# Optimization experiments

Hardware: AMD Instinct MI355X
Metric: run time of the kernel (lower is better)

Reference implementation:

```python
import jax, jax.numpy as jnp
import numpy as np

B, S, IN, H = 16, 1024, 1024, 1024

def setup_inputs() -> dict:
    key = jax.random.key(0)
    k1, k2 = jax.random.split(key)
    x = jax.random.normal(k1, (B, S, IN), dtype=jnp.float32)
    # xavier_uniform with gain sqrt(2) over shape [2H, IN]
    limit = np.sqrt(2.0) * np.sqrt(6.0 / (2 * H + IN))
    W = jax.random.uniform(k2, (2 * H, IN), dtype=jnp.float32, minval=-limit, maxval=limit)
    return {"x": x, "W": W}

def reference(x, W):
    # i = x @ W.T -> [B, S, 2H]; split into key/value pre-activations
    i = jnp.einsum('bsi,oi->bso', x, W)
    ik, iv = jnp.split(i, 2, axis=2)          # each [B, S, H]
    mem0 = jnp.zeros((x.shape[0], H, H), dtype=x.dtype)

    def step(mem, kv):
        ik_t, iv_t = kv                        # [B, H] each
        k = jax.nn.relu(ik_t)
        v = jax.nn.relu(iv_t)
        # Hebbian plasticity rule: delta_mem = key outer val
        mem = mem + jnp.einsum('bk,bv->bkv', k, v)
        return mem, (k, v)

    # scan over time: move seq axis to front
    kv_seq = (jnp.swapaxes(ik, 0, 1), jnp.swapaxes(iv, 0, 1))  # [S, B, H]
    mem, (keys, vals) = jax.lax.scan(step, mem0, kv_seq)
    keys = jnp.swapaxes(keys, 0, 1)            # [B, S, H]
    vals = jnp.swapaxes(vals, 0, 1)
    return mem, keys, vals
```

## Files before the change

kernel.cpp:

```cpp
#include <hip/hip_runtime.h>

#define B_  16
#define S_  1024
#define IN_ 1024
#define H_  1024
#define N1  (2*H_)
#define M1  (B_*S_)
#define K1  IN_
#define XN  (M1*IN_)
#define WN  (N1*IN_)
#define LDG 1024

#define BM  256
#define BN  256
#define BK  64
#define CP  257

#define USZ  8192
#define ASZ  16384
#define TBUF 32768

typedef __attribute__((ext_vector_type(8))) short  short8;
typedef __attribute__((ext_vector_type(4))) float  floatx4;

__device__ __forceinline__ unsigned short f2bf(float f) {
    unsigned int u = __float_as_uint(f);
    u += 0x7fffu + ((u >> 16) & 1u);
    return (unsigned short)(u >> 16);
}

#define GLDS16(gp, lp) __builtin_amdgcn_global_load_lds(                      \
    (const __attribute__((address_space(1))) void*)(gp),                      \
    (__attribute__((address_space(3))) void*)(lp), 16, 0, 0)

#define WAITVM(N) { asm volatile("s_waitcnt vmcnt(" #N ")" ::: "memory");     \
                    __builtin_amdgcn_s_barrier();                             \
                    __builtin_amdgcn_sched_barrier(0); }

__global__ __launch_bounds__(256) void convert_kernel(
    const float* __restrict__ x, const float* __restrict__ W,
    unsigned short* __restrict__ xb, unsigned short* __restrict__ Wb)
{
    size_t i = ((size_t)blockIdx.x * 256 + threadIdx.x) * 8;
    const float* src;
    unsigned short* dst;
    if (i < (size_t)XN) { src = x + i; dst = xb + i; }
    else                { src = W + (i - XN); dst = Wb + (i - XN); }
    float4 a = *(const float4*)(src);
    float4 b = *(const float4*)(src + 4);
    ushort4 p = { f2bf(a.x), f2bf(a.y), f2bf(a.z), f2bf(a.w) };
    ushort4 q = { f2bf(b.x), f2bf(b.y), f2bf(b.z), f2bf(b.w) };
    *(ushort4*)(dst)     = p;
    *(ushort4*)(dst + 4) = q;
}

__device__ __forceinline__ void stage_u(
    const unsigned short* Ag, const unsigned short* Bg,
    unsigned short* buf, int op, int kh, int kt, int wave, int lane)
{
    const unsigned short* src = op ? Bg : Ag;
    unsigned short* dst = buf + op * ASZ + kh * USZ;
#pragma unroll
    for (int h = 0; h < 2; ++h) {
        int e   = (wave * 2 + h) * 64 + lane;
        int row = e >> 2, p = e & 3;
        int c   = p ^ (row & 3);
        GLDS16(src + (size_t)row * LDG + kt + kh * 32 + c * 8,
               dst + (wave * 2 + h) * 512);
    }
}

__device__ __forceinline__ void half_tile(
    const unsigned short* bufc, floatx4 (&acc)[8][4], int kc,
    const unsigned short* Ag, const unsigned short* Bg,
    unsigned short* bufn, int ktn, bool st,
    int wave, int lane, int wmw, int wnw, int quad, int r)
{
    const unsigned short* cA = bufc + kc * USZ;
    const unsigned short* cB = bufc + ASZ + kc * USZ;
    const int sw = (quad ^ (r & 3)) * 8;
    short8 bfr[4];
#pragma unroll
    for (int j = 0; j < 4; ++j)
        bfr[j] = *(const short8*)(cB + (wnw + j * 16 + r) * 32 + sw);
#pragma unroll
    for (int mh = 0; mh < 2; ++mh) {
        short8 af[4];
#pragma unroll
        for (int i = 0; i < 4; ++i)
            af[i] = *(const short8*)(cA + (wmw + (mh * 4 + i) * 16 + r) * 32 + sw);
        if (st) stage_u(Ag, Bg, bufn, mh, kc, ktn, wave, lane);
        __builtin_amdgcn_s_setprio(1);
#pragma unroll
        for (int i = 0; i < 4; ++i)
#pragma unroll
            for (int j = 0; j < 4; ++j)
                acc[mh * 4 + i][j] = __builtin_amdgcn_mfma_f32_16x16x32_bf16(
                    af[i], bfr[j], acc[mh * 4 + i][j], 0, 0, 0);
        __builtin_amdgcn_s_setprio(0);
    }
}

__device__ __forceinline__ void gemm_core(
    const unsigned short* Ag, const unsigned short* Bg,
    unsigned short* lds, floatx4 (&acc)[8][4], int wave, int lane)
{
    const int quad = lane >> 4, r = lane & 15;
    const int wmw  = (wave >> 2) * 128;
    const int wnw  = (wave & 3) * 64;

    stage_u(Ag, Bg, lds, 0, 0, 0, wave, lane);
    stage_u(Ag, Bg, lds, 1, 0, 0, wave, lane);
    stage_u(Ag, Bg, lds, 0, 1, 0, wave, lane);
    stage_u(Ag, Bg, lds, 1, 1, 0, wave, lane);

    for (int t = 0; t < 15; ++t) {
        unsigned short* bufc = lds + (t & 1) * TBUF;
        unsigned short* bufn = lds + ((t + 1) & 1) * TBUF;
        const int ktn = (t + 1) * BK;
        WAITVM(4)
        half_tile(bufc, acc, 0, Ag, Bg, bufn, ktn, true, wave, lane, wmw, wnw, quad, r);
        WAITVM(4)
        half_tile(bufc, acc, 1, Ag, Bg, bufn, ktn, true, wave, lane, wmw, wnw, quad, r);
    }
    {
        unsigned short* bufc = lds + TBUF;
        WAITVM(4)
        half_tile(bufc, acc, 0, Ag, Bg, bufc, 0, false, wave, lane, wmw, wnw, quad, r);
        WAITVM(0)
        half_tile(bufc, acc, 1, Ag, Bg, bufc, 0, false, wave, lane, wmw, wnw, quad, r);
    }
    __syncthreads();
}

__global__ __launch_bounds__(512, 2) void gemm1_kernel(
    const unsigned short* __restrict__ xb, const unsigned short* __restrict__ Wb,
    float* __restrict__ out,
    unsigned short* __restrict__ kT, unsigned short* __restrict__ vT)
{
    __shared__ unsigned short lds[65536];

    const int tid  = threadIdx.x;
    const int wave = tid >> 6, lane = tid & 63;
    const int quad = lane >> 4, r = lane & 15;
    const int wmw  = (wave >> 2) * 128;
    const int wnw  = (wave & 3) * 64;

    const int L   = blockIdx.x;
    const int xcd = L & 7, s = L >> 3;
    const int mt  = xcd * 8 + (s >> 3);
    const int nt  = s & 7;
    const int m0  = mt * BM, n0 = nt * BN;

    const unsigned short* Ag = xb + (size_t)m0 * K1;
    const unsigned short* Bg = Wb + (size_t)n0 * K1;

    floatx4 acc[8][4] = {};
    gemm_core(Ag, Bg, lds, acc, wave, lane);

    const bool isKeys = (nt < 4);
    float* outKV    = out + (isKeys ? (size_t)M1 * H_ : (size_t)2 * M1 * H_);
    const int ncol0 = isKeys ? n0 : (n0 - 1024);

#pragma unroll
    for (int f = 0; f < 8; ++f)
#pragma unroll
        for (int j = 0; j < 4; ++j)
#pragma unroll
            for (int d = 0; d < 4; ++d) {
                int row_l = wmw + f * 16 + quad * 4 + d;
                int col_l = wnw + j * 16 + r;
                outKV[(size_t)(m0 + row_l) * H_ + ncol0 + col_l] =
                    fmaxf(acc[f][j][d], 0.0f);
            }

    unsigned short* wsT = isKeys ? kT : vT;
    const int b  = m0 >> 10;
    const int s0 = m0 & 1023;
    unsigned short* dstB = wsT + (size_t)b * H_ * S_ + (size_t)ncol0 * S_ + s0;

#pragma unroll
    for (int ch = 0; ch < 2; ++ch) {
        if ((wave >> 2) == ch) {
#pragma unroll
            for (int f = 0; f < 8; ++f)
#pragma unroll
                for (int j = 0; j < 4; ++j)
#pragma unroll
                    for (int d = 0; d < 4; ++d) {
                        int lrow = f * 16 + quad * 4 + d;
                        int col  = wnw + j * 16 + r;
                        lds[lrow * CP + col] = f2bf(fmaxf(acc[f][j][d], 0.0f));
                    }
        }
        __syncthreads();
#pragma unroll
        for (int it = 0; it < 16; ++it) {
            int o   = it * 512 + tid;
            int n_l = o >> 5;
            int m4  = (o & 31) * 4;
            ushort4 v;
            v.x = lds[(m4 + 0) * CP + n_l];
            v.y = lds[(m4 + 1) * CP + n_l];
            v.z = lds[(m4 + 2) * CP + n_l];
            v.w = lds[(m4 + 3) * CP + n_l];
            *(ushort4*)(dstB + (size_t)n_l * S_ + ch * 128 + m4) = v;
        }
        __syncthreads();
    }
}

__global__ __launch_bounds__(512, 2) void gemm2_kernel(
    const unsigned short* __restrict__ kT, const unsigned short* __restrict__ vT,
    float* __restrict__ mem)
{
    __shared__ unsigned short lds[65536];

    const int tid  = threadIdx.x;
    const int wave = tid >> 6, lane = tid & 63;
    const int quad = lane >> 4, r = lane & 15;
    const int wmw  = (wave >> 2) * 128;
    const int wnw  = (wave & 3) * 64;

    const int L   = blockIdx.x;
    const int xcd = L & 7, s = L >> 3;
    const int b   = xcd * 2 + (s >> 4);
    const int tt  = s & 15;
    const int m0  = (tt >> 2) * BM;
    const int n0  = (tt & 3) * BN;

    const unsigned short* Ag = kT + (size_t)b * H_ * S_ + (size_t)m0 * S_;
    const unsigned short* Bg = vT + (size_t)b * H_ * S_ + (size_t)n0 * S_;

    floatx4 acc[8][4] = {};
    gemm_core(Ag, Bg, lds, acc, wave, lane);

    float* outb = mem + (size_t)b * H_ * H_;
#pragma unroll
    for (int f = 0; f < 8; ++f)
#pragma unroll
        for (int j = 0; j < 4; ++j)
#pragma unroll
            for (int d = 0; d < 4; ++d) {
                int row_l = wmw + f * 16 + quad * 4 + d;
                int col_l = wnw + j * 16 + r;
                outb[(size_t)(m0 + row_l) * H_ + n0 + col_l] = acc[f][j][d];
            }
}

extern "C" void kernel_launch(void* const* d_in, const int* in_sizes, int n_in,
                              void* d_out, int out_size, void* d_ws, size_t ws_size,
                              hipStream_t stream) {
    const float* x = (const float*)d_in[0];
    const float* W = (const float*)d_in[1];
    float* out = (float*)d_out;

    unsigned short* xb = (unsigned short*)d_out;
    unsigned short* Wb = xb + (size_t)XN;

    unsigned short* kT = (unsigned short*)d_ws;
    unsigned short* vT = kT + (size_t)B_ * H_ * S_;

    convert_kernel<<<dim3((XN + WN) / 2048), dim3(256), 0, stream>>>(x, W, xb, Wb);

    gemm1_kernel<<<dim3(512), dim3(512), 0, stream>>>(xb, Wb, out, kT, vT);

    gemm2_kernel<<<dim3(256), dim3(512), 0, stream>>>(kT, vT, out);
}
```

Measured before the change: 350.8 us.

## Restructure GEMM main loop into barrier-bracketed phases with early prefetch issue

Rewrites the bf16 MFMA GEMM inner loop into four explicit phases per K-tile. Each phase issues the next tile's global-to-LDS loads before its barrier, waits on vmcnt only where the data is needed, and separates LDS reads from MFMA with lgkmcnt waits and closing barriers. The aim is to overlap global loads with compute more deterministically and keep waves in lockstep so MFMA bursts line up. It adds more barriers per tile, which can cost time if they serialize the waves.

```diff
diff --git a/kernel.cpp b/kernel.cpp
--- a/kernel.cpp
+++ b/kernel.cpp
@@ -9,7 +9,6 @@
 #define K1  IN_
 #define XN  (M1*IN_)
 #define WN  (N1*IN_)
-#define LDG 1024
 
 #define BM  256
 #define BN  256
@@ -33,9 +32,21 @@
     (const __attribute__((address_space(1))) void*)(gp),                      \
     (__attribute__((address_space(3))) void*)(lp), 16, 0, 0)
 
-#define WAITVM(N) { asm volatile("s_waitcnt vmcnt(" #N ")" ::: "memory");     \
-                    __builtin_amdgcn_s_barrier();                             \
-                    __builtin_amdgcn_sched_barrier(0); }
+#define OPEN_VM6 { asm volatile("s_waitcnt vmcnt(6)" ::: "memory");           \
+                   __builtin_amdgcn_s_barrier();                              \
+                   __builtin_amdgcn_sched_barrier(0); }
+#define OPEN_VM4 { asm volatile("s_waitcnt vmcnt(4)" ::: "memory");           \
+                   __builtin_amdgcn_s_barrier();                              \
+                   __builtin_amdgcn_sched_barrier(0); }
+#define OPEN_VM0 { asm volatile("s_waitcnt vmcnt(0)" ::: "memory");           \
+                   __builtin_amdgcn_s_barrier();                              \
+                   __builtin_amdgcn_sched_barrier(0); }
+#define OPEN_BAR { __builtin_amdgcn_s_barrier();                              \
+                   __builtin_amdgcn_sched_barrier(0); }
+#define CLOSE_BAR { __builtin_amdgcn_sched_barrier(0);                        \
+                    __builtin_amdgcn_s_barrier(); }
+#define LGKM0 { asm volatile("s_waitcnt lgkmcnt(0)" ::: "memory");            \
+                __builtin_amdgcn_sched_barrier(0); }
 
 __global__ __launch_bounds__(256) void convert_kernel(
     const float* __restrict__ x, const float* __restrict__ W,
@@ -65,39 +76,8 @@
         int e   = (wave * 2 + h) * 64 + lane;
         int row = e >> 2, p = e & 3;
         int c   = p ^ (row & 3);
-        GLDS16(src + (size_t)row * LDG + kt + kh * 32 + c * 8,
+        GLDS16(src + (size_t)row * 1024 + kt + kh * 32 + c * 8,
                dst + (wave * 2 + h) * 512);
-    }
-}
-
-__device__ __forceinline__ void half_tile(
-    const unsigned short* bufc, floatx4 (&acc)[8][4], int kc,
-    const unsigned short* Ag, const unsigned short* Bg,
-    unsigned short* bufn, int ktn, bool st,
-    int wave, int lane, int wmw, int wnw, int quad, int r)
-{
-    const unsigned short* cA = bufc + kc * USZ;
-    const unsigned short* cB = bufc + ASZ + kc * USZ;
-    const int sw = (quad ^ (r & 3)) * 8;
-    short8 bfr[4];
-#pragma unroll
-    for (int j = 0; j < 4; ++j)
-        bfr[j] = *(const short8*)(cB + (wnw + j * 16 + r) * 32 + sw);
-#pragma unroll
-    for (int mh = 0; mh < 2; ++mh) {
-        short8 af[4];
-#pragma unroll
-        for (int i = 0; i < 4; ++i)
-            af[i] = *(const short8*)(cA + (wmw + (mh * 4 + i) * 16 + r) * 32 + sw);
-        if (st) stage_u(Ag, Bg, bufn, mh, kc, ktn, wave, lane);
-        __builtin_amdgcn_s_setprio(1);
-#pragma unroll
-        for (int i = 0; i < 4; ++i)
-#pragma unroll
-            for (int j = 0; j < 4; ++j)
-                acc[mh * 4 + i][j] = __builtin_amdgcn_mfma_f32_16x16x32_bf16(
-                    af[i], bfr[j], acc[mh * 4 + i][j], 0, 0, 0);
-        __builtin_amdgcn_s_setprio(0);
     }
 }
 
@@ -108,29 +88,86 @@
     const int quad = lane >> 4, r = lane & 15;
     const int wmw  = (wave >> 2) * 128;
     const int wnw  = (wave & 3) * 64;
+    const int sw   = (quad ^ (r & 3)) * 8;
+
+    short8 af[4], bfr[4];
+
+#define READ_B(cur_, kh_)                                                     \
+    _Pragma("unroll") for (int j = 0; j < 4; ++j)                             \
+        bfr[j] = *(const short8*)((cur_) + ASZ + (kh_) * USZ                  \
+                                  + (wnw + j * 16 + r) * 32 + sw);
+#define READ_A(cur_, kh_, mh_)                                                \
+    _Pragma("unroll") for (int i = 0; i < 4; ++i)                             \
+        af[i] = *(const short8*)((cur_) + (kh_) * USZ                         \
+                                 + (wmw + ((mh_) * 4 + i) * 16 + r) * 32 + sw);
+#define MFMA16(mh_)                                                           \
+    __builtin_amdgcn_s_setprio(1);                                            \
+    _Pragma("unroll") for (int i = 0; i < 4; ++i)                             \
+        _Pragma("unroll") for (int j = 0; j < 4; ++j)                         \
+            acc[(mh_) * 4 + i][j] = __builtin_amdgcn_mfma_f32_16x16x32_bf16(  \
+                af[i], bfr[j], acc[(mh_) * 4 + i][j], 0, 0, 0);               \
+    __builtin_amdgcn_s_setprio(0);
 
     stage_u(Ag, Bg, lds, 0, 0, 0, wave, lane);
     stage_u(Ag, Bg, lds, 1, 0, 0, wave, lane);
     stage_u(Ag, Bg, lds, 0, 1, 0, wave, lane);
     stage_u(Ag, Bg, lds, 1, 1, 0, wave, lane);
 
-    for (int t = 0; t < 15; ++t) {
-        unsigned short* bufc = lds + (t & 1) * TBUF;
-        unsigned short* bufn = lds + ((t + 1) & 1) * TBUF;
-        const int ktn = (t + 1) * BK;
-        WAITVM(4)
-        half_tile(bufc, acc, 0, Ag, Bg, bufn, ktn, true, wave, lane, wmw, wnw, quad, r);
-        WAITVM(4)
-        half_tile(bufc, acc, 1, Ag, Bg, bufn, ktn, true, wave, lane, wmw, wnw, quad, r);
+    for (int T = 0; T < 15; ++T) {
+        unsigned short* cur = lds + (T & 1) * TBUF;
+        unsigned short* nxt = lds + ((T + 1) & 1) * TBUF;
+        const int ktn = (T + 1) * BK;
+        stage_u(Ag, Bg, nxt, 0, 0, ktn, wave, lane);
+        OPEN_VM6
+        READ_B(cur, 0) READ_A(cur, 0, 0)
+        LGKM0
+        MFMA16(0)
+        CLOSE_BAR
+        stage_u(Ag, Bg, nxt, 1, 0, ktn, wave, lane);
+        OPEN_BAR
+        READ_A(cur, 0, 1)
+        LGKM0
+        MFMA16(1)
+        CLOSE_BAR
+        stage_u(Ag, Bg, nxt, 0, 1, ktn, wave, lane);
+        OPEN_VM6
+        READ_B(cur, 1) READ_A(cur, 1, 0)
+        LGKM0
+        MFMA16(0)
+        CLOSE_BAR
+        stage_u(Ag, Bg, nxt, 1, 1, ktn, wave, lane);
+        OPEN_BAR
+        READ_A(cur, 1, 1)
+        LGKM0
+        MFMA16(1)
+        CLOSE_BAR
     }
     {
-        unsigned short* bufc = lds + TBUF;
-        WAITVM(4)
-        half_tile(bufc, acc, 0, Ag, Bg, bufc, 0, false, wave, lane, wmw, wnw, quad, r);
-        WAITVM(0)
-        half_tile(bufc, acc, 1, Ag, Bg, bufc, 0, false, wave, lane, wmw, wnw, quad, r);
+        unsigned short* cur = lds + TBUF;
+        OPEN_VM4
+        READ_B(cur, 0) READ_A(cur, 0, 0)
+        LGKM0
+        MFMA16(0)
+        CLOSE_BAR
+        OPEN_BAR
+        READ_A(cur, 0, 1)
+        LGKM0
+        MFMA16(1)
+        CLOSE_BAR
+        OPEN_VM0
+        READ_B(cur, 1) READ_A(cur, 1, 0)
+        LGKM0
+        MFMA16(0)
+        CLOSE_BAR
+        OPEN_BAR
+        READ_A(cur, 1, 1)
+        LGKM0
+        MFMA16(1)
     }
     __syncthreads();
+#undef READ_B
+#undef READ_A
+#undef MFMA16
 }
 
 __global__ __launch_bounds__(512, 2) void gemm1_kernel(
```

Result: no change. 357.2 us (+1.8%).
